# Performance work log

Measured on AMD Instinct MI355X. Metric: run time of the kernel, lower is better.

Reference implementation:

```python
import jax, jax.numpy as jnp
import numpy as np

EPS = 1e-05   # CE eps
T = 3         # Newton-Schulz iterations
G = 4         # num_groups = 256 // 64
D = 64        # num_channels per group
LN_EPS = 1e-05


def setup_inputs() -> dict:
    key = jax.random.key(0)
    k0, k1, k2 = jax.random.split(key, 3)
    X = jax.random.normal(k0, (32, 256, 64, 64), dtype=jnp.float32)
    fc1_w = jax.random.normal(k1, (64, 256), dtype=jnp.float32) * 0.05
    ln_g = jnp.ones((64,), dtype=jnp.float32)
    ln_b = jnp.zeros((64,), dtype=jnp.float32)
    fc2_w = jax.random.normal(k2, (256, 64), dtype=jnp.float32) * 0.05
    x_weight = jnp.zeros((1,), dtype=jnp.float32)
    return {"X": X, "fc1_w": fc1_w, "ln_g": ln_g, "ln_b": ln_b,
            "fc2_w": fc2_w, "x_weight": x_weight}


def reference(X, fc1_w, ln_g, ln_b, fc2_w, x_weight):
    N, C, H, W = X.shape
    # ---- AdaptiveReweight (training branch) ----
    x_var = jnp.var(X.reshape(N, C, -1), axis=-1, ddof=1)          # [N, C], unbiased like torch.var
    h = x_var @ fc1_w.T                                            # [N, C//4]
    mu = h.mean(-1, keepdims=True)
    var = h.var(-1, keepdims=True)                                 # LayerNorm: biased variance
    h = (h - mu) / jnp.sqrt(var + LN_EPS) * ln_g + ln_b
    h = jax.nn.relu(h)
    y = jax.nn.sigmoid(h @ fc2_w.T)                                # [N, C]
    scale = jnp.sqrt(x_var.mean())                                 # scalar (training)
    xin = (y / scale)[:, :, None, None] * X                        # [N, C, H, W]
    # ---- group whitening (training branch, momentum=0 so buffers unused) ----
    x = jnp.transpose(X, (1, 0, 2, 3)).reshape(G, D, -1)           # [G, d, m], channel-major
    m = x.shape[-1]
    mean = x.mean(-1, keepdims=True)
    xc = x - mean
    I = jnp.eye(D, dtype=X.dtype)
    # modern torch.baddbmm keyword semantics: beta*input + alpha*(b1@b2)
    Sigma = (1.0 / m) * I + EPS * jnp.einsum('gdm,gem->gde', xc, xc)
    rTr = 1.0 / jnp.trace(Sigma, axis1=1, axis2=2)[:, None, None]  # (Sigma*I).sum = trace
    Sigma_N = Sigma * rTr
    P = jnp.broadcast_to(I, (G, D, D))
    for _ in range(T):
        P3 = P @ P @ P
        P = -0.5 * P + 1.5 * (P3 @ Sigma_N)
    xn = P @ x                                                     # note: original multiplies un-centered x
    Xn = jnp.transpose(xn.reshape(C, N, H, W), (1, 0, 2, 3))
    w = jax.nn.sigmoid(x_weight)[0]
    return w * Xn + (1.0 - w) * xin
```

## Files before the change

### kernel.cpp

```cpp
#include <hip/hip_runtime.h>

#define EPSC    1e-5f
#define LNEPS   1e-5f

typedef __attribute__((ext_vector_type(8))) short  short8;
typedef __attribute__((ext_vector_type(4))) float  floatx4;

static __device__ __forceinline__ unsigned short f2bf(float f){
  union { float f; unsigned int u; } v; v.f = f;
  unsigned int u = v.u;
  u += 0x7FFFu + ((u >> 16) & 1u);
  return (unsigned short)(u >> 16);
}
static __device__ __forceinline__ float bf2f(unsigned short h){
  union { unsigned int u; float f; } v; v.u = ((unsigned int)h) << 16;
  return v.f;
}

__global__ __launch_bounds__(256) void k_stats_gram(
    const float* __restrict__ X, float* __restrict__ S1p,
    float* __restrict__ S2p, float* __restrict__ gramP)
{
  const int half = blockIdx.x, g = blockIdx.y, n = blockIdx.z;
  const int t  = threadIdx.x;
  const int ch = t >> 2, f4 = t & 3;
  __shared__ unsigned short lt[64][88];

  const float* rowb = X + (size_t)(n*256 + g*64 + ch)*4096 + half*2048;

  float4 buf[4];
  #pragma unroll
  for (int i = 0; i < 4; ++i)
    buf[i] = *(const float4*)(rowb + (4*i + f4)*4);

  float s1 = 0.f, s2 = 0.f;
  floatx4 acc[4];
  #pragma unroll
  for (int i = 0; i < 4; ++i) acc[i] = (floatx4){0.f, 0.f, 0.f, 0.f};

  const int wv = t >> 6;
  const int l15 = t & 15, q = (t & 63) >> 4;

  for (int tile = 0; tile < 32; ++tile){
    #pragma unroll
    for (int i = 0; i < 4; ++i){
      float4 v = buf[i];
      s1 += (v.x + v.y) + (v.z + v.w);
      s2 += v.x*v.x + v.y*v.y + v.z*v.z + v.w*v.w;
      ushort4 b;
      b.x = f2bf(v.x); b.y = f2bf(v.y); b.z = f2bf(v.z); b.w = f2bf(v.w);
      *(ushort4*)&lt[ch][(4*i + f4)*4] = b;
    }
    __syncthreads();
    if (tile < 31){
      const float* nb = rowb + (tile + 1)*64;
      #pragma unroll
      for (int i = 0; i < 4; ++i)
        buf[i] = *(const float4*)(nb + (4*i + f4)*4);
    }
    #pragma unroll
    for (int k0 = 0; k0 < 64; k0 += 32){
      short8 af = *(const short8*)&lt[16*wv + l15][k0 + q*8];
      #pragma unroll
      for (int t4 = 0; t4 < 4; ++t4){
        short8 bf = *(const short8*)&lt[16*t4 + l15][k0 + q*8];
        acc[t4] = __builtin_amdgcn_mfma_f32_16x16x32_bf16(af, bf, acc[t4], 0, 0, 0);
      }
    }
    __syncthreads();
  }

  s1 += __shfl_down(s1, 2); s1 += __shfl_down(s1, 1);
  s2 += __shfl_down(s2, 2); s2 += __shfl_down(s2, 1);
  const int blk = n*8 + g*2 + half;
  if (f4 == 0){ S1p[blk*64 + ch] = s1; S2p[blk*64 + ch] = s2; }

  float* gp = gramP + (size_t)blk*4096;
  #pragma unroll
  for (int t4 = 0; t4 < 4; ++t4)
    #pragma unroll
    for (int r = 0; r < 4; ++r)
      gp[(16*wv + 4*q + r)*64 + 16*t4 + l15] = acc[t4][r];
}

__global__ __launch_bounds__(256) void k_reduce(
    const float* __restrict__ gramP, const float* __restrict__ S1p,
    const float* __restrict__ S2p,
    float* __restrict__ SigmaS, float* __restrict__ xvar,
    float* __restrict__ cmean, float* __restrict__ vsum)
{
  const int t = threadIdx.x, b = blockIdx.x;
  if (b < 64){
    const int idx = b*256 + t;
    const int g = idx >> 12, e = idx & 4095;
    const float* p = gramP + (size_t)(g*2)*4096 + e;
    float s = 0.f;
    for (int n = 0; n < 32; ++n){ s += p[0] + p[4096]; p += 8*4096; }
    SigmaS[idx] = s;
  } else {
    __shared__ float red[256];
    float lsum = 0.f;
    #pragma unroll
    for (int i = 0; i < 32; ++i){
      const int idx = t + i*256;
      const int n = idx >> 8, c = idx & 255;
      const int base = (n*8 + (c >> 6)*2)*64 + (c & 63);
      const float s1 = S1p[base] + S1p[base + 64];
      const float s2 = S2p[base] + S2p[base + 64];
      const float v = (s2 - s1*s1*(1.f/4096.f)) * (1.f/4095.f);
      xvar[idx] = v; lsum += v;
    }
    red[t] = lsum;
    __syncthreads();
    for (int s = 128; s > 0; s >>= 1){
      if (t < s) red[t] += red[t + s];
      __syncthreads();
    }
    if (t == 0) vsum[0] = red[0];
    {
      const int g = t >> 6, cc = t & 63;
      float s = 0.f;
      for (int n = 0; n < 32; ++n){
        const float* p = S1p + (n*8 + g*2)*64 + cc;
        s += p[0] + p[64];
      }
      cmean[t] = s * (1.f/131072.f);
    }
  }
}

#define STR 72

__global__ __launch_bounds__(256) void k_mid2(
    const float* __restrict__ SigmaS, const float* __restrict__ cmean,
    const float* __restrict__ xvar, const float* __restrict__ vsum,
    const float* __restrict__ fc1_w, const float* __restrict__ ln_g,
    const float* __restrict__ ln_b, const float* __restrict__ fc2_w,
    const float* __restrict__ xw,
    float* __restrict__ Pw, float* __restrict__ aOut)
{
  __shared__ __align__(16) unsigned short us[6*64*STR];
  __shared__ float fbuf[512];
  const int t = threadIdx.x;
  const float wsig = 1.f / (1.f + __expf(-xw[0]));

  if (blockIdx.x < 4){
    const int g = blockIdx.x;
    const int w4 = t >> 6, l15 = t & 15, q = (t & 63) >> 4;
    unsigned short* SNh = us;
    unsigned short* SNl = us + 1*64*STR;
    unsigned short* Ph  = us + 2*64*STR;
    unsigned short* Pl_ = us + 3*64*STR;
    unsigned short* Th  = us + 4*64*STR;
    unsigned short* Tl  = us + 5*64*STR;
    float* cml = fbuf;
    float* rtr = fbuf + 64;

    if (t < 64) cml[t] = cmean[g*64 + t];
    __syncthreads();
    if (t < 64){
      const float cm = cml[t];
      float v = EPSC * (SigmaS[g*4096 + t*65] - 131072.f*cm*cm) + (1.f/131072.f);
      v += __shfl_xor(v, 32); v += __shfl_xor(v, 16);
      v += __shfl_xor(v, 8);  v += __shfl_xor(v, 4);
      v += __shfl_xor(v, 2);  v += __shfl_xor(v, 1);
      if (t == 0) rtr[0] = 1.f / v;
    }
    __syncthreads();
    const float rT = rtr[0];

    floatx4 Pf[4];
    #pragma unroll
    for (int nt = 0; nt < 4; ++nt){
      #pragma unroll
      for (int r = 0; r < 4; ++r){
        const int d = w4*16 + q*4 + r;
        const int e = nt*16 + l15;
        float sig = EPSC * (SigmaS[g*4096 + d*64 + e] - 131072.f*cml[d]*cml[e]);
        if (d == e) sig += (1.f/131072.f);
        const float sn = sig * rT;
        const unsigned short hi = f2bf(sn);
        SNh[d*STR + e] = hi;
        SNl[d*STR + e] = f2bf(sn - bf2f(hi));
        const float pv = (d == e) ? 1.f : 0.f;
        Pf[nt][r] = pv;
        Ph[d*STR + e] = f2bf(pv);
        Pl_[d*STR + e] = 0;
      }
    }
    __syncthreads();

    #define MM(AH, AL, BH, BL, OUT)                                            \
    {                                                                          \
      _Pragma("unroll")                                                        \
      for (int nt = 0; nt < 4; ++nt) OUT[nt] = (floatx4){0.f,0.f,0.f,0.f};     \
      _Pragma("unroll")                                                        \
      for (int ks = 0; ks < 2; ++ks){                                          \
        const int ko = ks*32 + q*8;                                            \
        short8 ah = *(const short8*)&AH[(w4*16 + l15)*STR + ko];               \
        short8 al = *(const short8*)&AL[(w4*16 + l15)*STR + ko];               \
        _Pragma("unroll")                                                      \
        for (int nt = 0; nt < 4; ++nt){                                        \
          short8 bh = *(const short8*)&BH[(nt*16 + l15)*STR + ko];             \
          short8 bl = *(const short8*)&BL[(nt*16 + l15)*STR + ko];             \
          OUT[nt] = __builtin_amdgcn_mfma_f32_16x16x32_bf16(ah, bh, OUT[nt], 0,0,0); \
          OUT[nt] = __builtin_amdgcn_mfma_f32_16x16x32_bf16(ah, bl, OUT[nt], 0,0,0); \
          OUT[nt] = __builtin_amdgcn_mfma_f32_16x16x32_bf16(al, bh, OUT[nt], 0,0,0); \
        }                                                                      \
      }                                                                        \
    }

    #define CONV(FR, H, L)                                                     \
    {                                                                          \
      _Pragma("unroll")                                                        \
      for (int nt = 0; nt < 4; ++nt){                                          \
        _Pragma("unroll")                                                      \
        for (int r = 0; r < 4; ++r){                                           \
          const int d = w4*16 + q*4 + r;                                       \
          const int e = nt*16 + l15;                                           \
          const float x = FR[nt][r];                                           \
          const unsigned short hi = f2bf(x);                                   \
          H[d*STR + e] = hi;                                                   \
          L[d*STR + e] = f2bf(x - bf2f(hi));                                   \
        }                                                                      \
      }                                                                        \
    }

    floatx4 Tf[4];
    for (int it = 0; it < 3; ++it){
      MM(Ph, Pl_, Ph, Pl_, Tf);
      __syncthreads();
      CONV(Tf, Th, Tl);
      __syncthreads();
      MM(Th, Tl, Ph, Pl_, Tf);
      __syncthreads();
      CONV(Tf, Th, Tl);
      __syncthreads();
      MM(Th, Tl, SNh, SNl, Tf);
      #pragma unroll
      for (int nt = 0; nt < 4; ++nt)
        #pragma unroll
        for (int r = 0; r < 4; ++r)
          Pf[nt][r] = -0.5f*Pf[nt][r] + 1.5f*Tf[nt][r];
      __syncthreads();
      if (it < 2){
        CONV(Pf, Ph, Pl_);
        __syncthreads();
      }
    }

    #pragma unroll
    for (int nt = 0; nt < 4; ++nt)
      #pragma unroll
      for (int r = 0; r < 4; ++r){
        const int d = w4*16 + q*4 + r;
        const int e = nt*16 + l15;
        Pw[g*4096 + d*64 + e] = wsig * Pf[nt][r];
      }
  } else {
    const int n = blockIdx.x - 4;
    const int lane = t & 63, w4 = t >> 6;
    float* xl  = fbuf;
    float* hb  = fbuf + 256;
    float* hnb = fbuf + 320;

    if (t < 64) *(float4*)&xl[t*4] = *(const float4*)&xvar[n*256 + t*4];
    __syncthreads();

    const float4 xv4 = *(const float4*)&xl[lane*4];
    #pragma unroll
    for (int it = 0; it < 16; ++it){
      const int j = w4*16 + it;
      const float4 wv = *(const float4*)&fc1_w[j*256 + lane*4];
      float v = xv4.x*wv.x + xv4.y*wv.y + xv4.z*wv.z + xv4.w*wv.w;
      v += __shfl_down(v, 32); v += __shfl_down(v, 16);
      v += __shfl_down(v, 8);  v += __shfl_down(v, 4);
      v += __shfl_down(v, 2);  v += __shfl_down(v, 1);
      if (lane == 0) hb[j] = v;
    }
    __syncthreads();

    if (t < 64){
      const float hv = hb[t];
      float s = hv, s2 = hv*hv;
      #pragma unroll
      for (int o = 32; o > 0; o >>= 1){
        s  += __shfl_xor(s,  o);
        s2 += __shfl_xor(s2, o);
      }
      const float mu = s * (1.f/64.f);
      const float var = s2 * (1.f/64.f) - mu*mu;
      float v = (hv - mu) * rsqrtf(var + LNEPS) * ln_g[t] + ln_b[t];
      hnb[t] = v > 0.f ? v : 0.f;
    }
    __syncthreads();

    const float scale = sqrtf(vsum[0] * (1.f/8192.f));
    const float ascl = (1.f - wsig) / scale;
    const int l15 = lane & 15, rgrp = lane >> 4;
    const float4 hn4 = *(const float4*)&hnb[l15*4];
    #pragma unroll
    for (int it = 0; it < 16; ++it){
      const int c = w4*64 + it*4 + rgrp;
      const float4 wv = *(const float4*)&fc2_w[c*64 + l15*4];
      float v = hn4.x*wv.x + hn4.y*wv.y + hn4.z*wv.z + hn4.w*wv.w;
      v += __shfl_down(v, 8); v += __shfl_down(v, 4);
      v += __shfl_down(v, 2); v += __shfl_down(v, 1);
      if (l15 == 0)
        aOut[n*256 + c] = ascl / (1.f + __expf(-v));
    }
  }
}

__global__ __launch_bounds__(256) void k_final(
    const float* __restrict__ X, const float* __restrict__ Pw,
    const float* __restrict__ aIn, float* __restrict__ out)
{
  const int bx = blockIdx.x, g = blockIdx.y, n = blockIdx.z;
  const int t = threadIdx.x;
  __shared__ float xt[64*132];
  __shared__ float Pl[4096];
  __shared__ float al[64];

  {
    const int ch = t >> 2, f4 = t & 3;
    const float* rowb = X + (size_t)(n*256 + g*64 + ch)*4096 + bx*128;
    float* ld = xt + ch*132;
    #pragma unroll
    for (int i = 0; i < 8; ++i){
      const int col = (4*i + f4)*4;
      *(float4*)(ld + col) = *(const float4*)(rowb + col);
    }
  }
  #pragma unroll
  for (int i = 0; i < 16; ++i)
    Pl[t + 256*i] = Pw[g*4096 + t + 256*i];
  if (t < 64) al[t] = aIn[n*256 + g*64 + t];
  __syncthreads();

  const int hwq = t & 31, og = t >> 5;
  const float* xcol = xt + hwq*4;
  float4 acc[8];
  #pragma unroll
  for (int dd = 0; dd < 8; ++dd){
    const int d = og*8 + dd;
    float4 xv = *(const float4*)(xcol + d*132);
    const float av = al[d];
    acc[dd].x = av*xv.x; acc[dd].y = av*xv.y; acc[dd].z = av*xv.z; acc[dd].w = av*xv.w;
  }
  for (int e4 = 0; e4 < 16; ++e4){
    float4 x0 = *(const float4*)(xcol + (e4*4 + 0)*132);
    float4 x1 = *(const float4*)(xcol + (e4*4 + 1)*132);
    float4 x2 = *(const float4*)(xcol + (e4*4 + 2)*132);
    float4 x3 = *(const float4*)(xcol + (e4*4 + 3)*132);
    #pragma unroll
    for (int dd = 0; dd < 8; ++dd){
      const int d = og*8 + dd;
      float4 p = *(const float4*)(Pl + d*64 + e4*4);
      acc[dd].x += p.x*x0.x + p.y*x1.x + p.z*x2.x + p.w*x3.x;
      acc[dd].y += p.x*x0.y + p.y*x1.y + p.z*x2.y + p.w*x3.y;
      acc[dd].z += p.x*x0.z + p.y*x1.z + p.z*x2.z + p.w*x3.z;
      acc[dd].w += p.x*x0.w + p.y*x1.w + p.z*x2.w + p.w*x3.w;
    }
  }
  float* ob = out + (size_t)(n*256 + g*64)*4096 + bx*128 + hwq*4;
  #pragma unroll
  for (int dd = 0; dd < 8; ++dd)
    *(float4*)(ob + (size_t)(og*8 + dd)*4096) = acc[dd];
}

extern "C" void kernel_launch(void* const* d_in, const int* in_sizes, int n_in,
                              void* d_out, int out_size, void* d_ws, size_t ws_size,
                              hipStream_t stream)
{
  const float* X     = (const float*)d_in[0];
  const float* fc1_w = (const float*)d_in[1];
  const float* ln_g  = (const float*)d_in[2];
  const float* ln_b  = (const float*)d_in[3];
  const float* fc2_w = (const float*)d_in[4];
  const float* xw    = (const float*)d_in[5];
  float* out = (float*)d_out;

  char* ws = (char*)d_ws;
  float* gramP  = (float*)ws;
  float* S1p    = (float*)(ws + 4194304);
  float* S2p    = (float*)(ws + 4259840);
  float* SigmaS = (float*)(ws + 4325376);
  float* Pwb    = (float*)(ws + 4390912);
  float* aB     = (float*)(ws + 4456448);
  float* xvarB  = (float*)(ws + 4489216);
  float* cmeanB = (float*)(ws + 4521984);
  float* vsumB  = (float*)(ws + 4523008);

  k_stats_gram<<<dim3(2, 4, 32), 256, 0, stream>>>(X, S1p, S2p, gramP);
  k_reduce<<<65, 256, 0, stream>>>(gramP, S1p, S2p, SigmaS, xvarB, cmeanB, vsumB);
  k_mid2<<<36, 256, 0, stream>>>(SigmaS, cmeanB, xvarB, vsumB,
                                 fc1_w, ln_g, ln_b, fc2_w, xw, Pwb, aB);
  k_final<<<dim3(32, 4, 32), 256, 0, stream>>>(X, Pwb, aB, out);
}
```

Before: 318.3 us.

## Split stats/Gram pass into quarters and restructure final projection with transposed P

The Gram/statistics kernel now splits each channel row into four chunks instead of two, doubling the block count from 256 to 512 so the read of X is spread over more CUs; the reduce kernel sums four partials per sample. The final kernel no longer stages P and the scale vector in shared memory. P is written transposed and each wave reads it directly from global memory as wave-uniform rows, while X is staged unpadded with coalesced loads, and each thread computes 16 output channels for 2 spatial positions, with a launch bound targeting higher occupancy. This trades more partial-sum traffic and a larger workspace for more parallelism and less LDS use and synchronisation in the memory-bound stages.

```diff
diff --git a/kernel.cpp b/kernel.cpp
--- a/kernel.cpp
+++ b/kernel.cpp
@@ -21,12 +21,12 @@
     const float* __restrict__ X, float* __restrict__ S1p,
     float* __restrict__ S2p, float* __restrict__ gramP)
 {
-  const int half = blockIdx.x, g = blockIdx.y, n = blockIdx.z;
+  const int q4 = blockIdx.x, g = blockIdx.y, n = blockIdx.z;
   const int t  = threadIdx.x;
   const int ch = t >> 2, f4 = t & 3;
   __shared__ unsigned short lt[64][88];
 
-  const float* rowb = X + (size_t)(n*256 + g*64 + ch)*4096 + half*2048;
+  const float* rowb = X + (size_t)(n*256 + g*64 + ch)*4096 + q4*1024;
 
   float4 buf[4];
   #pragma unroll
@@ -41,7 +41,7 @@
   const int wv = t >> 6;
   const int l15 = t & 15, q = (t & 63) >> 4;
 
-  for (int tile = 0; tile < 32; ++tile){
+  for (int tile = 0; tile < 16; ++tile){
     #pragma unroll
     for (int i = 0; i < 4; ++i){
       float4 v = buf[i];
@@ -52,7 +52,7 @@
       *(ushort4*)&lt[ch][(4*i + f4)*4] = b;
     }
     __syncthreads();
-    if (tile < 31){
+    if (tile < 15){
       const float* nb = rowb + (tile + 1)*64;
       #pragma unroll
       for (int i = 0; i < 4; ++i)
@@ -72,7 +72,7 @@
 
   s1 += __shfl_down(s1, 2); s1 += __shfl_down(s1, 1);
   s2 += __shfl_down(s2, 2); s2 += __shfl_down(s2, 1);
-  const int blk = n*8 + g*2 + half;
+  const int blk = n*16 + g*4 + q4;
   if (f4 == 0){ S1p[blk*64 + ch] = s1; S2p[blk*64 + ch] = s2; }
 
   float* gp = gramP + (size_t)blk*4096;
@@ -93,9 +93,12 @@
   if (b < 64){
     const int idx = b*256 + t;
     const int g = idx >> 12, e = idx & 4095;
-    const float* p = gramP + (size_t)(g*2)*4096 + e;
+    const float* p = gramP + (size_t)(g*4)*4096 + e;
     float s = 0.f;
-    for (int n = 0; n < 32; ++n){ s += p[0] + p[4096]; p += 8*4096; }
+    for (int n = 0; n < 32; ++n){
+      s += (p[0] + p[4096]) + (p[2*4096] + p[3*4096]);
+      p += 16*4096;
+    }
     SigmaS[idx] = s;
   } else {
     __shared__ float red[256];
@@ -104,9 +107,9 @@
     for (int i = 0; i < 32; ++i){
       const int idx = t + i*256;
       const int n = idx >> 8, c = idx & 255;
-      const int base = (n*8 + (c >> 6)*2)*64 + (c & 63);
-      const float s1 = S1p[base] + S1p[base + 64];
-      const float s2 = S2p[base] + S2p[base + 64];
+      const int base = (n*16 + (c >> 6)*4)*64 + (c & 63);
+      const float s1 = (S1p[base] + S1p[base+64]) + (S1p[base+128] + S1p[base+192]);
+      const float s2 = (S2p[base] + S2p[base+64]) + (S2p[base+128] + S2p[base+192]);
       const float v = (s2 - s1*s1*(1.f/4096.f)) * (1.f/4095.f);
       xvar[idx] = v; lsum += v;
     }
@@ -121,8 +124,8 @@
       const int g = t >> 6, cc = t & 63;
       float s = 0.f;
       for (int n = 0; n < 32; ++n){
-        const float* p = S1p + (n*8 + g*2)*64 + cc;
-        s += p[0] + p[64];
+        const float* p = S1p + (n*16 + g*4)*64 + cc;
+        s += (p[0] + p[64]) + (p[128] + p[192]);
       }
       cmean[t] = s * (1.f/131072.f);
     }
@@ -137,7 +140,7 @@
     const float* __restrict__ fc1_w, const float* __restrict__ ln_g,
     const float* __restrict__ ln_b, const float* __restrict__ fc2_w,
     const float* __restrict__ xw,
-    float* __restrict__ Pw, float* __restrict__ aOut)
+    float* __restrict__ PwT, float* __restrict__ aOut)
 {
   __shared__ __align__(16) unsigned short us[6*64*STR];
   __shared__ float fbuf[512];
@@ -255,7 +258,7 @@
       for (int r = 0; r < 4; ++r){
         const int d = w4*16 + q*4 + r;
         const int e = nt*16 + l15;
-        Pw[g*4096 + d*64 + e] = wsig * Pf[nt][r];
+        PwT[g*4096 + e*64 + d] = wsig * Pf[nt][r];
       }
   } else {
     const int n = blockIdx.x - 4;
@@ -312,61 +315,64 @@
   }
 }
 
-__global__ __launch_bounds__(256) void k_final(
-    const float* __restrict__ X, const float* __restrict__ Pw,
+__global__ __launch_bounds__(256, 4) void k_final(
+    const float* __restrict__ X, const float* __restrict__ PwT,
     const float* __restrict__ aIn, float* __restrict__ out)
 {
   const int bx = blockIdx.x, g = blockIdx.y, n = blockIdx.z;
   const int t = threadIdx.x;
-  __shared__ float xt[64*132];
-  __shared__ float Pl[4096];
-  __shared__ float al[64];
-
+  __shared__ float xt[64*128];
+
+  const float* Xg = X + (size_t)(n*256 + g*64)*4096 + bx*128;
   {
-    const int ch = t >> 2, f4 = t & 3;
-    const float* rowb = X + (size_t)(n*256 + g*64 + ch)*4096 + bx*128;
-    float* ld = xt + ch*132;
-    #pragma unroll
-    for (int i = 0; i < 8; ++i){
-      const int col = (4*i + f4)*4;
-      *(float4*)(ld + col) = *(const float4*)(rowb + col);
-    }
-  }
+    float4 v[8];
+    #pragma unroll
+    for (int c = 0; c < 8; ++c){
+      const int id = c*256 + t;
+      const int e = id >> 5;
+      const int hw4 = (id & 31) << 2;
+      v[c] = *(const float4*)(Xg + (size_t)e*4096 + hw4);
+    }
+    #pragma unroll
+    for (int c = 0; c < 8; ++c){
+      const int id = c*256 + t;
+      *(float4*)&xt[id << 2] = v[c];
+    }
+  }
+  __syncthreads();
+
+  const int wv = __builtin_amdgcn_readfirstlane(t >> 6);
+  const int lane = t & 63;
+  const float* Pr = PwT + g*4096 + wv*16;
+  const float* ar = aIn + n*256 + g*64 + wv*16;
+
+  float2 acc[16];
   #pragma unroll
-  for (int i = 0; i < 16; ++i)
-    Pl[t + 256*i] = Pw[g*4096 + t + 256*i];
-  if (t < 64) al[t] = aIn[n*256 + g*64 + t];
-  __syncthreads();
-
-  const int hwq = t & 31, og = t >> 5;
-  const float* xcol = xt + hwq*4;
-  float4 acc[8];
+  for (int dd = 0; dd < 16; ++dd){
+    const int d = wv*16 + dd;
+    const float2 xv = *(const float2*)&xt[d*128 + lane*2];
+    const float av = ar[dd];
+    acc[dd].x = av * xv.x; acc[dd].y = av * xv.y;
+  }
+
+  #pragma unroll 2
+  for (int e = 0; e < 64; ++e){
+    const float2 xv = *(const float2*)&xt[e*128 + lane*2];
+    const float* pe = Pr + e*64;
+    #pragma unroll
+    for (int d4 = 0; d4 < 4; ++d4){
+      const float4 p = *(const float4*)(pe + d4*4);
+      acc[d4*4+0].x += p.x*xv.x; acc[d4*4+0].y += p.x*xv.y;
+      acc[d4*4+1].x += p.y*xv.x; acc[d4*4+1].y += p.y*xv.y;
+      acc[d4*4+2].x += p.z*xv.x; acc[d4*4+2].y += p.z*xv.y;
+      acc[d4*4+3].x += p.w*xv.x; acc[d4*4+3].y += p.w*xv.y;
+    }
+  }
+
+  float* ob = out + (size_t)(n*256 + g*64 + wv*16)*4096 + bx*128 + lane*2;
   #pragma unroll
-  for (int dd = 0; dd < 8; ++dd){
-    const int d = og*8 + dd;
-    float4 xv = *(const float4*)(xcol + d*132);
-    const float av = al[d];
-    acc[dd].x = av*xv.x; acc[dd].y = av*xv.y; acc[dd].z = av*xv.z; acc[dd].w = av*xv.w;
-  }
-  for (int e4 = 0; e4 < 16; ++e4){
-    float4 x0 = *(const float4*)(xcol + (e4*4 + 0)*132);
-    float4 x1 = *(const float4*)(xcol + (e4*4 + 1)*132);
-    float4 x2 = *(const float4*)(xcol + (e4*4 + 2)*132);
-    float4 x3 = *(const float4*)(xcol + (e4*4 + 3)*132);
-    #pragma unroll
-    for (int dd = 0; dd < 8; ++dd){
-      const int d = og*8 + dd;
-      float4 p = *(const float4*)(Pl + d*64 + e4*4);
-      acc[dd].x += p.x*x0.x + p.y*x1.x + p.z*x2.x + p.w*x3.x;
-      acc[dd].y += p.x*x0.y + p.y*x1.y + p.z*x2.y + p.w*x3.y;
-      acc[dd].z += p.x*x0.z + p.y*x1.z + p.z*x2.z + p.w*x3.z;
-      acc[dd].w += p.x*x0.w + p.y*x1.w + p.z*x2.w + p.w*x3.w;
-    }
-  }
-  float* ob = out + (size_t)(n*256 + g*64)*4096 + bx*128 + hwq*4;
-  #pragma unroll
-  for (int dd = 0; dd < 8; ++dd)
-    *(float4*)(ob + (size_t)(og*8 + dd)*4096) = acc[dd];
+  for (int dd = 0; dd < 16; ++dd)
+    *(float2*)(ob + (size_t)dd*4096) = acc[dd];
 }
 
 extern "C" void kernel_launch(void* const* d_in, const int* in_sizes, int n_in,
@@ -383,18 +389,18 @@
 
   char* ws = (char*)d_ws;
   float* gramP  = (float*)ws;
-  float* S1p    = (float*)(ws + 4194304);
-  float* S2p    = (float*)(ws + 4259840);
-  float* SigmaS = (float*)(ws + 4325376);
-  float* Pwb    = (float*)(ws + 4390912);
-  float* aB     = (float*)(ws + 4456448);
-  float* xvarB  = (float*)(ws + 4489216);
-  float* cmeanB = (float*)(ws + 4521984);
-  float* vsumB  = (float*)(ws + 4523008);
-
-  k_stats_gram<<<dim3(2, 4, 32), 256, 0, stream>>>(X, S1p, S2p, gramP);
+  float* S1p    = (float*)(ws + 8388608);
+  float* S2p    = (float*)(ws + 8519680);
+  float* SigmaS = (float*)(ws + 8650752);
+  float* PwTb   = (float*)(ws + 8716288);
+  float* aB     = (float*)(ws + 8781824);
+  float* xvarB  = (float*)(ws + 8814592);
+  float* cmeanB = (float*)(ws + 8847360);
+  float* vsumB  = (float*)(ws + 8848384);
+
+  k_stats_gram<<<dim3(4, 4, 32), 256, 0, stream>>>(X, S1p, S2p, gramP);
   k_reduce<<<65, 256, 0, stream>>>(gramP, S1p, S2p, SigmaS, xvarB, cmeanB, vsumB);
   k_mid2<<<36, 256, 0, stream>>>(SigmaS, cmeanB, xvarB, vsumB,
-                                 fc1_w, ln_g, ln_b, fc2_w, xw, Pwb, aB);
-  k_final<<<dim3(32, 4, 32), 256, 0, stream>>>(X, Pwb, aB, out);
-}
+                                 fc1_w, ln_g, ln_b, fc2_w, xw, PwTb, aB);
+  k_final<<<dim3(32, 4, 32), 256, 0, stream>>>(X, PwTb, aB, out);
+}
```

Measured after the change: 323.3 us. Within noise of the previous version (+1.6%).
